# Kernel tuning notes

Measured on AMD Instinct MI355X. Metric: run time of the kernel, lower is better.

The kernel has to match this reference:

```python
import jax, jax.numpy as jnp
import numpy as np

DIM = 1024
MULTIPLE_OF = 256
NUM_EXPERTS = 8
TOP_K = 2
T = 2048  # flattened tokens


def _hidden_dim(dim: int, multiple_of: int) -> int:
    h = 4 * dim
    h = int(2 * h / 3)
    return multiple_of * ((h + multiple_of - 1) // multiple_of)

HIDDEN = _hidden_dim(DIM, MULTIPLE_OF)  # 2816


def setup_inputs() -> dict:
    key = jax.random.key(0)
    k_x, k_idx, k1, k2, k3 = jax.random.split(key, 5)
    x = jax.random.normal(k_x, (T, DIM), dtype=jnp.float32)
    expert_indices = jax.random.randint(k_idx, (T, TOP_K), 0, NUM_EXPERTS, dtype=jnp.int32)
    # parameters, matching nn.Parameter(torch.randn(E, H, D))
    w1 = jax.random.normal(k1, (NUM_EXPERTS, HIDDEN, DIM), dtype=jnp.float32)
    w2 = jax.random.normal(k2, (NUM_EXPERTS, HIDDEN, DIM), dtype=jnp.float32)
    w3 = jax.random.normal(k3, (NUM_EXPERTS, HIDDEN, DIM), dtype=jnp.float32)
    return {"x": x, "expert_indices": expert_indices, "w1": w1, "w2": w2, "w3": w3}


def reference(x, expert_indices, w1, w2, w3):
    # Same math as the torch module, but instead of materializing the
    # per-token gathered weights [T, A, H, D] (which the original does and
    # which blows up memory), we compute the SwiGLU FFN for ALL experts via
    # dense GEMMs and gather the selected experts' outputs per token.
    # Gather commutes with the per-expert linear maps, so math is identical.
    x1_all = jax.nn.silu(jnp.einsum('td,ehd->teh', x, w1))  # [T, E, H]
    x3_all = jnp.einsum('td,ehd->teh', x, w3)               # [T, E, H]
    g_all = x1_all * x3_all                                  # [T, E, H]
    out_all = jnp.einsum('teh,ehd->ted', g_all, w2)          # [T, E, D]
    # select top_k experts per token -> [T, A, D]
    idx = expert_indices[:, :, None].astype(jnp.int32)       # [T, A, 1]
    return jnp.take_along_axis(out_all, idx, axis=1)
```

## Files before the change

### kernel.cpp

```cpp
#include <hip/hip_runtime.h>

#define NTOK 2048
#define NEXP 8
#define TOPK 2
#define NITEM 4096
#define DIM 1024
#define HID 2816
#define CAP 4096
#define LDP 72

typedef unsigned short u16;
typedef __bf16 bf16x8 __attribute__((ext_vector_type(8)));
typedef float f32x4 __attribute__((ext_vector_type(4)));

__device__ __forceinline__ u16 f2bf(float f) {
  unsigned u = __float_as_uint(f);
  return (u16)((u + 0x7FFFu + ((u >> 16) & 1u)) >> 16);
}
__device__ __forceinline__ unsigned pk2(float a, float b) {
  return (unsigned)f2bf(a) | ((unsigned)f2bf(b) << 16);
}
__device__ __forceinline__ void async16(const void* g, void* l) {
  __builtin_amdgcn_global_load_lds(
      (const __attribute__((address_space(1))) unsigned int*)g,
      (__attribute__((address_space(3))) unsigned int*)l, 16, 0, 0);
}
__device__ __forceinline__ const bf16x8* fragpA(const u16* base, int row, int ko) {
  int byte = ((row << 7) + (ko << 1)) ^ ((row & 7) << 4);
  return (const bf16x8*)((const char*)base + byte);
}
__device__ __forceinline__ const bf16x8* fragpB(const u16* base, int row, int kg) {
  int byte = (row << 6) + ((kg << 4) ^ (((row >> 1) & 3) << 4));
  return (const bf16x8*)((const char*)base + byte);
}
__device__ __forceinline__ void cvst8(const float4& a, const float4& b, void* dst) {
  union { __bf16 h[8]; uint4 q; } u;
  u.h[0] = (__bf16)a.x; u.h[1] = (__bf16)a.y; u.h[2] = (__bf16)a.z; u.h[3] = (__bf16)a.w;
  u.h[4] = (__bf16)b.x; u.h[5] = (__bf16)b.y; u.h[6] = (__bf16)b.z; u.h[7] = (__bf16)b.w;
  *(uint4*)dst = u.q;
}

__global__ void zero8(int* counts) {
  if (threadIdx.x < NEXP) counts[threadIdx.x] = 0;
}

__global__ void bucket(const int* __restrict__ ei, int* counts, int* lists) {
  int item = blockIdx.x * 256 + threadIdx.x;
  if (item < NITEM) {
    int e = ei[item] & 7;
    int pos = atomicAdd(&counts[e], 1);
    if (pos < CAP) lists[e * CAP + pos] = item;
  }
}

__global__ __launch_bounds__(256) void cvt8(const float* __restrict__ src,
                                            u16* __restrict__ dst, int n8) {
  int i = blockIdx.x * 256 + threadIdx.x;
  if (i >= n8) return;
  float4 v0 = *(const float4*)(src + (size_t)i * 8);
  float4 v1 = *(const float4*)(src + (size_t)i * 8 + 4);
  uint4 u;
  u.x = pk2(v0.x, v0.y); u.y = pk2(v0.z, v0.w);
  u.z = pk2(v1.x, v1.y); u.w = pk2(v1.z, v1.w);
  *(uint4*)(dst + (size_t)i * 8) = u;
}

__global__ __launch_bounds__(256) void tw2(const float* __restrict__ w2, u16* __restrict__ w2t) {
  __shared__ float tile[64][65];
  const int e = blockIdx.z;
  const int h0 = blockIdx.y * 64;
  const int d0 = blockIdx.x * 64;
  const int tid = threadIdx.x;
  const int r = tid >> 4, c = (tid & 15) * 4;
  const float* src = w2 + (size_t)e * HID * DIM;
#pragma unroll
  for (int p = 0; p < 4; ++p) {
    float4 v = *(const float4*)(src + (size_t)(h0 + p * 16 + r) * DIM + d0 + c);
    tile[p * 16 + r][c] = v.x;
    tile[p * 16 + r][c + 1] = v.y;
    tile[p * 16 + r][c + 2] = v.z;
    tile[p * 16 + r][c + 3] = v.w;
  }
  __syncthreads();
  u16* dst = w2t + (size_t)e * DIM * HID;
#pragma unroll
  for (int p = 0; p < 4; ++p) {
    int dd = p * 16 + r;
    uint2 pkv;
    pkv.x = pk2(tile[c][dd], tile[c + 1][dd]);
    pkv.y = pk2(tile[c + 2][dd], tile[c + 3][dd]);
    *(uint2*)(dst + (size_t)(d0 + dd) * HID + h0 + c) = pkv;
  }
}


__global__ __launch_bounds__(256, 2) void gemm1H(
    const u16* __restrict__ xb, const float* __restrict__ w1,
    const float* __restrict__ w3, const int* __restrict__ counts,
    const int* __restrict__ lists, u16* __restrict__ G) {
  __shared__ __align__(16) u16 As[2][256 * 32];
  __shared__ __align__(16) u16 B1s[2][64 * 32];
  __shared__ __align__(16) u16 B3s[2][64 * 32];
  __shared__ int toks[256];

  const int e = blockIdx.z;
  int cnt = counts[e];
  if ((unsigned)cnt > CAP) cnt = 0;
  const int m0 = blockIdx.y * 256;
  if (m0 >= cnt) return;
  const int n0 = blockIdx.x * 64;
  const int tid = threadIdx.x;

  {
    int r = m0 + tid;
    int it = lists[e * CAP + (r < cnt ? r : 0)];
    toks[tid] = ((unsigned)it < NITEM) ? it : 0;
  }
  __syncthreads();

  const int lane = tid & 63;
  const int wrow = (tid >> 6) * 64;
  const int lr = lane & 15;
  const int kg = lane >> 4;

  const int prow = tid >> 2;
  const int q = tid & 3;
  const int ascol = (q ^ ((prow >> 1) & 3)) * 8;
  const u16* xs[4];
#pragma unroll
  for (int p = 0; p < 4; ++p)
    xs[p] = xb + (size_t)(toks[p * 64 + prow] >> 1) * DIM + ascol;

  const int br = prow;
  const float* w1p = w1 + ((size_t)e * HID + n0 + br) * DIM + q * 8;
  const float* w3p = w3 + ((size_t)e * HID + n0 + br) * DIM + q * 8;
  const int bby = (br << 6) + ((q << 4) ^ (((br >> 1) & 3) << 4));

  float4 b1r[2][2], b3r[2][2];
  f32x4 acc1[4][4] = {};
  f32x4 acc3[4][4] = {};

#define KCL(k) ((k) < DIM ? (k) : (DIM - 32))
#define G1_LOADB(set, k)                                  \
  {                                                       \
    b1r[set][0] = *(const float4*)(w1p + (k));            \
    b1r[set][1] = *(const float4*)(w1p + (k) + 4);        \
    b3r[set][0] = *(const float4*)(w3p + (k));            \
    b3r[set][1] = *(const float4*)(w3p + (k) + 4);        \
  }
#define G1_STGA(buf, k)                                   \
  {                                                       \
    char* aD = (char*)As[buf] + tid * 16;                 \
    async16(xs[0] + (k), aD);                             \
    async16(xs[1] + (k), aD + 4096);                      \
    async16(xs[2] + (k), aD + 8192);                      \
    async16(xs[3] + (k), aD + 12288);                     \
  }
#define G1_WRITEB(buf, set)                                   \
  {                                                           \
    cvst8(b1r[set][0], b1r[set][1], (char*)B1s[buf] + bby);   \
    cvst8(b3r[set][0], b3r[set][1], (char*)B3s[buf] + bby);   \
  }
#define G1_COMP(cb)                                                          \
  {                                                                          \
    bf16x8 a[4];                                                             \
    _Pragma("unroll") for (int m = 0; m < 4; ++m)                            \
        a[m] = *fragpB(As[cb], wrow + m * 16 + lr, kg);                      \
    _Pragma("unroll") for (int n = 0; n < 4; ++n) {                          \
      bf16x8 b1 = *fragpB(B1s[cb], n * 16 + lr, kg);                         \
      bf16x8 b3 = *fragpB(B3s[cb], n * 16 + lr, kg);                         \
      _Pragma("unroll") for (int m = 0; m < 4; ++m) {                        \
        acc1[m][n] = __builtin_amdgcn_mfma_f32_16x16x32_bf16(a[m], b1, acc1[m][n], 0, 0, 0); \
        acc3[m][n] = __builtin_amdgcn_mfma_f32_16x16x32_bf16(a[m], b3, acc3[m][n], 0, 0, 0); \
      }                                                                      \
    }                                                                        \
  }
#define G1_ITER(i, cb)                                               \
  {                                                                  \
    G1_STGA(cb ^ 1, KCL(32 * ((i) + 1)));                            \
    G1_WRITEB(cb ^ 1, cb ^ 1);              \
    __builtin_amdgcn_sched_barrier(0);                               \
    G1_LOADB(cb, KCL(32 * ((i) + 2)));                               \
    __builtin_amdgcn_sched_barrier(0);                               \
    G1_COMP(cb);                                                     \
    asm volatile("s_waitcnt vmcnt(4) lgkmcnt(0)" ::: "memory");      \
    __builtin_amdgcn_sched_barrier(0);                               \
    __builtin_amdgcn_s_barrier();                                    \
    __builtin_amdgcn_sched_barrier(0);                               \
  }

  G1_LOADB(0, 0);
  __builtin_amdgcn_sched_barrier(0);
  G1_STGA(0, 0);
  __builtin_amdgcn_sched_barrier(0);
  G1_LOADB(1, 32);
  asm volatile("s_waitcnt vmcnt(4)" ::: "memory");
  __builtin_amdgcn_sched_barrier(0);
  G1_WRITEB(0, 0);
  asm volatile("s_waitcnt lgkmcnt(0)" ::: "memory");
  __builtin_amdgcn_sched_barrier(0);
  __builtin_amdgcn_s_barrier();
  __builtin_amdgcn_sched_barrier(0);

  for (int i = 0; i < 32; i += 2) {
    G1_ITER(i, 0);
    G1_ITER(i + 1, 1);
  }
#undef G1_ITER
#undef G1_COMP
#undef G1_WRITEB
#undef G1_STGA
#undef G1_LOADB
#undef KCL

#pragma unroll
  for (int m = 0; m < 4; ++m) {
#pragma unroll
    for (int r = 0; r < 4; ++r) {
      const int row = wrow + m * 16 + kg * 4 + r;
      if (m0 + row < cnt) {
        const int it = toks[row];
        u16* gp = G + (size_t)it * HID + n0 + lr;
#pragma unroll
        for (int n = 0; n < 4; ++n) {
          float v1 = acc1[m][n][r];
          float v3 = acc3[m][n][r];
          float s = v1 / (1.f + __expf(-v1)) * v3;
          gp[n * 16] = f2bf(s);
        }
      }
    }
  }
}

__global__ __launch_bounds__(256, 3) void gemm2F(
    const u16* __restrict__ G, const u16* __restrict__ w2t,
    const int* __restrict__ counts, const int* __restrict__ lists,
    float* __restrict__ out) {
  __shared__ __align__(16) u16 As[2][128 * 64];
  __shared__ __align__(16) u16 Bs[2][64 * 64];
  __shared__ int toks[128];

  const int e = blockIdx.z;
  int cnt = counts[e];
  if ((unsigned)cnt > CAP) cnt = 0;
  const int m0 = blockIdx.y * 128;
  if (m0 >= cnt) return;
  const int n0 = blockIdx.x * 64;
  const int tid = threadIdx.x;

  if (tid < 128) {
    int r = m0 + tid;
    int it = lists[e * CAP + (r < cnt ? r : 0)];
    toks[tid] = ((unsigned)it < NITEM) ? it : 0;
  }
  __syncthreads();

  const int lane = tid & 63;
  const int wid = tid >> 6;
  const int wr = (wid >> 1) * 64;
  const int wc = (wid & 1) * 32;
  const int lr = lane & 15;
  const int kg = lane >> 4;

  const int srow = tid >> 3;
  const int scol = ((tid & 7) ^ (srow & 7)) * 8;

  const u16* as0 = G + (size_t)toks[srow] * HID + scol;
  const u16* as1 = G + (size_t)toks[32 + srow] * HID + scol;
  const u16* as2 = G + (size_t)toks[64 + srow] * HID + scol;
  const u16* as3 = G + (size_t)toks[96 + srow] * HID + scol;
  const u16* bs0 = w2t + ((size_t)e * DIM + n0 + srow) * HID + scol;
  const u16* bs1 = bs0 + (size_t)32 * HID;

  f32x4 acc[4][2] = {};

#define STG2(buf, k)                          \
  {                                           \
    char* aD = (char*)As[buf] + tid * 16;     \
    char* bD = (char*)Bs[buf] + tid * 16;     \
    async16(as0 + (k), aD);                   \
    async16(as1 + (k), aD + 4096);            \
    async16(as2 + (k), aD + 8192);            \
    async16(as3 + (k), aD + 12288);           \
    async16(bs0 + (k), bD);                   \
    async16(bs1 + (k), bD + 4096);            \
  }

  STG2(0, 0);
  __syncthreads();

  int cur = 0;
  for (int k0 = 0; k0 < HID; k0 += 64) {
    if (k0 + 64 < HID) STG2(cur ^ 1, k0 + 64);
    const u16* Ab = As[cur];
    const u16* Bb = Bs[cur];
#pragma unroll
    for (int kk = 0; kk < 2; ++kk) {
      const int ko = kk * 32 + kg * 8;
      bf16x8 a[4], b[2];
#pragma unroll
      for (int m = 0; m < 4; ++m) a[m] = *fragpA(Ab, wr + m * 16 + lr, ko);
#pragma unroll
      for (int n = 0; n < 2; ++n) b[n] = *fragpA(Bb, wc + n * 16 + lr, ko);
#pragma unroll
      for (int n = 0; n < 2; ++n)
#pragma unroll
        for (int m = 0; m < 4; ++m)
          acc[m][n] = __builtin_amdgcn_mfma_f32_16x16x32_bf16(a[m], b[n], acc[m][n], 0, 0, 0);
    }
    __syncthreads();
    cur ^= 1;
  }
#undef STG2

#pragma unroll
  for (int m = 0; m < 4; ++m) {
#pragma unroll
    for (int r = 0; r < 4; ++r) {
      const int row = wr + m * 16 + kg * 4 + r;
      if (m0 + row < cnt) {
        const int it = toks[row];
        float* op = out + (size_t)it * DIM + n0 + wc + lr;
#pragma unroll
        for (int n = 0; n < 2; ++n)
          op[n * 16] = acc[m][n][r];
      }
    }
  }
}


__global__ __launch_bounds__(256, 2) void gemm1B(
    const float* __restrict__ x, const float* __restrict__ w1,
    const float* __restrict__ w3, const int* __restrict__ counts,
    const int* __restrict__ lists, u16* __restrict__ G) {
  __shared__ __align__(16) u16 As[128 * LDP];
  __shared__ __align__(16) u16 B1s[128 * LDP];
  __shared__ __align__(16) u16 B3s[128 * LDP];
  __shared__ int toks[128];

  const int e = blockIdx.z;
  int cnt = counts[e];
  if ((unsigned)cnt > CAP) cnt = 0;
  const int m0 = blockIdx.y * 128;
  if (m0 >= cnt) return;
  const int n0 = blockIdx.x * 128;
  const int tid = threadIdx.x;

  if (tid < 128) {
    int r = m0 + tid;
    int it = lists[e * CAP + (r < cnt ? r : 0)];
    toks[tid] = ((unsigned)it < NITEM) ? it : 0;
  }
  __syncthreads();

  const int lane = tid & 63;
  const int wr = ((tid >> 7) & 1) * 64;
  const int wc = ((tid >> 6) & 1) * 64;
  const int lr = lane & 15;
  const int kg = lane >> 4;
  const int arow = tid >> 3;
  const int c8 = (tid & 7) * 8;

  const float* xsrc[4];
#pragma unroll
  for (int p = 0; p < 4; ++p)
    xsrc[p] = x + (size_t)(toks[p * 32 + arow] >> 1) * DIM + c8;
  const float* w1p = w1 + ((size_t)e * HID + n0 + arow) * DIM + c8;
  const float* w3p = w3 + ((size_t)e * HID + n0 + arow) * DIM + c8;

  f32x4 acc1[4][4] = {};
  f32x4 acc3[4][4] = {};

  for (int k0 = 0; k0 < DIM; k0 += 64) {
#pragma unroll
    for (int p = 0; p < 4; ++p) {
      float4 v0 = *(const float4*)(xsrc[p] + k0);
      float4 v1 = *(const float4*)(xsrc[p] + k0 + 4);
      uint4 u;
      u.x = pk2(v0.x, v0.y); u.y = pk2(v0.z, v0.w);
      u.z = pk2(v1.x, v1.y); u.w = pk2(v1.z, v1.w);
      *(uint4*)&As[(p * 32 + arow) * LDP + c8] = u;
    }
#pragma unroll
    for (int p = 0; p < 4; ++p) {
      float4 v0 = *(const float4*)(w1p + (size_t)(p * 32) * DIM + k0);
      float4 v1 = *(const float4*)(w1p + (size_t)(p * 32) * DIM + k0 + 4);
      uint4 u;
      u.x = pk2(v0.x, v0.y); u.y = pk2(v0.z, v0.w);
      u.z = pk2(v1.x, v1.y); u.w = pk2(v1.z, v1.w);
      *(uint4*)&B1s[(p * 32 + arow) * LDP + c8] = u;
      v0 = *(const float4*)(w3p + (size_t)(p * 32) * DIM + k0);
      v1 = *(const float4*)(w3p + (size_t)(p * 32) * DIM + k0 + 4);
      u.x = pk2(v0.x, v0.y); u.y = pk2(v0.z, v0.w);
      u.z = pk2(v1.x, v1.y); u.w = pk2(v1.z, v1.w);
      *(uint4*)&B3s[(p * 32 + arow) * LDP + c8] = u;
    }
    __syncthreads();
#pragma unroll
    for (int kk = 0; kk < 2; ++kk) {
      const int ko = kk * 32 + kg * 8;
      bf16x8 a[4];
#pragma unroll
      for (int m = 0; m < 4; ++m)
        a[m] = *(const bf16x8*)&As[(wr + m * 16 + lr) * LDP + ko];
#pragma unroll
      for (int n = 0; n < 4; ++n) {
        bf16x8 b1 = *(const bf16x8*)&B1s[(wc + n * 16 + lr) * LDP + ko];
        bf16x8 b3 = *(const bf16x8*)&B3s[(wc + n * 16 + lr) * LDP + ko];
#pragma unroll
        for (int m = 0; m < 4; ++m) {
          acc1[m][n] = __builtin_amdgcn_mfma_f32_16x16x32_bf16(a[m], b1, acc1[m][n], 0, 0, 0);
          acc3[m][n] = __builtin_amdgcn_mfma_f32_16x16x32_bf16(a[m], b3, acc3[m][n], 0, 0, 0);
        }
      }
    }
    __syncthreads();
  }

#pragma unroll
  for (int m = 0; m < 4; ++m) {
#pragma unroll
    for (int r = 0; r < 4; ++r) {
      const int row = wr + m * 16 + kg * 4 + r;
      if (m0 + row < cnt) {
        const int it = toks[row];
        u16* gp = G + (size_t)it * HID + n0 + wc + lr;
#pragma unroll
        for (int n = 0; n < 4; ++n) {
          float v1 = acc1[m][n][r];
          float v3 = acc3[m][n][r];
          float s = v1 / (1.f + __expf(-v1)) * v3;
          gp[n * 16] = f2bf(s);
        }
      }
    }
  }
}

__global__ __launch_bounds__(256, 2) void gemm2B(
    const u16* __restrict__ G, const float* __restrict__ w2,
    const int* __restrict__ counts, const int* __restrict__ lists,
    float* __restrict__ out) {
  __shared__ __align__(16) u16 As[128 * LDP];
  __shared__ __align__(16) u16 Bs[128 * LDP];
  __shared__ int toks[128];

  const int e = blockIdx.z;
  int cnt = counts[e];
  if ((unsigned)cnt > CAP) cnt = 0;
  const int m0 = blockIdx.y * 128;
  if (m0 >= cnt) return;
  const int n0 = blockIdx.x * 128;
  const int tid = threadIdx.x;

  if (tid < 128) {
    int r = m0 + tid;
    int it = lists[e * CAP + (r < cnt ? r : 0)];
    toks[tid] = ((unsigned)it < NITEM) ? it : 0;
  }
  __syncthreads();

  const int lane = tid & 63;
  const int wr = ((tid >> 7) & 1) * 64;
  const int wc = ((tid >> 6) & 1) * 64;
  const int lr = lane & 15;
  const int kg = lane >> 4;
  const int arow = tid >> 3;
  const int c8 = (tid & 7) * 8;
  const int brow = tid >> 5;
  const int d4 = (tid & 31) * 4;

  const u16* asrc[4];
#pragma unroll
  for (int p = 0; p < 4; ++p)
    asrc[p] = G + (size_t)toks[p * 32 + arow] * HID + c8;
  const float* bsrc = w2 + ((size_t)e * HID) * DIM + n0 + d4;

  f32x4 acc[4][4] = {};

  for (int k0 = 0; k0 < HID; k0 += 64) {
#pragma unroll
    for (int p = 0; p < 4; ++p) {
      uint4 u = *(const uint4*)(asrc[p] + k0);
      *(uint4*)&As[(p * 32 + arow) * LDP + c8] = u;
    }
#pragma unroll
    for (int p = 0; p < 8; ++p) {
      const int hl = p * 8 + brow;
      float4 v = *(const float4*)(bsrc + (size_t)(k0 + hl) * DIM);
      Bs[(d4 + 0) * LDP + hl] = f2bf(v.x);
      Bs[(d4 + 1) * LDP + hl] = f2bf(v.y);
      Bs[(d4 + 2) * LDP + hl] = f2bf(v.z);
      Bs[(d4 + 3) * LDP + hl] = f2bf(v.w);
    }
    __syncthreads();
#pragma unroll
    for (int kk = 0; kk < 2; ++kk) {
      const int ko = kk * 32 + kg * 8;
      bf16x8 a[4];
#pragma unroll
      for (int m = 0; m < 4; ++m)
        a[m] = *(const bf16x8*)&As[(wr + m * 16 + lr) * LDP + ko];
#pragma unroll
      for (int n = 0; n < 4; ++n) {
        bf16x8 b = *(const bf16x8*)&Bs[(wc + n * 16 + lr) * LDP + ko];
#pragma unroll
        for (int m = 0; m < 4; ++m)
          acc[m][n] = __builtin_amdgcn_mfma_f32_16x16x32_bf16(a[m], b, acc[m][n], 0, 0, 0);
      }
    }
    __syncthreads();
  }

#pragma unroll
  for (int m = 0; m < 4; ++m) {
#pragma unroll
    for (int r = 0; r < 4; ++r) {
      const int row = wr + m * 16 + kg * 4 + r;
      if (m0 + row < cnt) {
        const int it = toks[row];
        float* op = out + (size_t)it * DIM + n0 + wc + lr;
#pragma unroll
        for (int n = 0; n < 4; ++n)
          op[n * 16] = acc[m][n][r];
      }
    }
  }
}

extern "C" void kernel_launch(void* const* d_in, const int* in_sizes, int n_in,
                              void* d_out, int out_size, void* d_ws, size_t ws_size,
                              hipStream_t stream) {
  (void)in_sizes; (void)n_in; (void)out_size;
  const float* x  = (const float*)d_in[0];
  const int*   ei = (const int*)d_in[1];
  const float* w1 = (const float*)d_in[2];
  const float* w2 = (const float*)d_in[3];
  const float* w3 = (const float*)d_in[4];
  float* out = (float*)d_out;

  char* ws = (char*)d_ws;

  const size_t oG = 0;
  const size_t oXB = 23068672u;
  const size_t oW2T = oXB + 4194304u;
  const size_t oCNT = oW2T + 46137344u;
  const size_t oLST = oCNT + 64u;
  const size_t needA = oLST + 131072u;

  if (ws_size >= needA) {
    u16* G      = (u16*)(ws + oG);
    u16* xb     = (u16*)(ws + oXB);
    u16* w2t    = (u16*)(ws + oW2T);
    int* counts = (int*)(ws + oCNT);
    int* lists  = (int*)(ws + oLST);

    zero8<<<1, 64, 0, stream>>>(counts);
    bucket<<<NITEM / 256, 256, 0, stream>>>(ei, counts, lists);
    cvt8<<<(NTOK * DIM / 8) / 256, 256, 0, stream>>>(x, xb, NTOK * DIM / 8);
    gemm1H<<<dim3(HID / 64, CAP / 256, NEXP), 256, 0, stream>>>(xb, w1, w3, counts, lists, G);
    tw2<<<dim3(DIM / 64, HID / 64, NEXP), 256, 0, stream>>>(w2, w2t);
    gemm2F<<<dim3(DIM / 64, CAP / 128, NEXP), 256, 0, stream>>>(G, w2t, counts, lists, out);
  } else {
    u16* G      = (u16*)ws;
    int* counts = (int*)(ws + 23068672u);
    int* lists  = (int*)(ws + 23068736u);

    zero8<<<1, 64, 0, stream>>>(counts);
    bucket<<<NITEM / 256, 256, 0, stream>>>(ei, counts, lists);
    gemm1B<<<dim3(HID / 128, CAP / 128, NEXP), 256, 0, stream>>>(x, w1, w3, counts, lists, G);
    gemm2B<<<dim3(DIM / 128, CAP / 128, NEXP), 256, 0, stream>>>(G, w2, counts, lists, out);
  }
}
```

Before: 211.4 us.

## Fuse w2 transpose-convert into second GEMM and triple-buffer first GEMM A tiles

```diff
diff --git a/kernel.cpp b/kernel.cpp
--- a/kernel.cpp
+++ b/kernel.cpp
@@ -65,50 +65,27 @@
   *(uint4*)(dst + (size_t)i * 8) = u;
 }
 
-__global__ __launch_bounds__(256) void tw2(const float* __restrict__ w2, u16* __restrict__ w2t) {
-  __shared__ float tile[64][65];
-  const int e = blockIdx.z;
-  const int h0 = blockIdx.y * 64;
-  const int d0 = blockIdx.x * 64;
-  const int tid = threadIdx.x;
-  const int r = tid >> 4, c = (tid & 15) * 4;
-  const float* src = w2 + (size_t)e * HID * DIM;
-#pragma unroll
-  for (int p = 0; p < 4; ++p) {
-    float4 v = *(const float4*)(src + (size_t)(h0 + p * 16 + r) * DIM + d0 + c);
-    tile[p * 16 + r][c] = v.x;
-    tile[p * 16 + r][c + 1] = v.y;
-    tile[p * 16 + r][c + 2] = v.z;
-    tile[p * 16 + r][c + 3] = v.w;
-  }
-  __syncthreads();
-  u16* dst = w2t + (size_t)e * DIM * HID;
-#pragma unroll
-  for (int p = 0; p < 4; ++p) {
-    int dd = p * 16 + r;
-    uint2 pkv;
-    pkv.x = pk2(tile[c][dd], tile[c + 1][dd]);
-    pkv.y = pk2(tile[c + 2][dd], tile[c + 3][dd]);
-    *(uint2*)(dst + (size_t)(d0 + dd) * HID + h0 + c) = pkv;
-  }
-}
-
-
-__global__ __launch_bounds__(256, 2) void gemm1H(
+
+__global__ __launch_bounds__(256, 2) void gemm1I(
     const u16* __restrict__ xb, const float* __restrict__ w1,
     const float* __restrict__ w3, const int* __restrict__ counts,
     const int* __restrict__ lists, u16* __restrict__ G) {
-  __shared__ __align__(16) u16 As[2][256 * 32];
+  __shared__ __align__(16) u16 As[3][256 * 32];
   __shared__ __align__(16) u16 B1s[2][64 * 32];
   __shared__ __align__(16) u16 B3s[2][64 * 32];
   __shared__ int toks[256];
 
-  const int e = blockIdx.z;
+  const int flat = blockIdx.x;
+  const int n_id = flat % 44;
+  const int t2 = flat / 44;
+  const int e = t2 & 7;
+  const int m_id = t2 >> 3;
+
   int cnt = counts[e];
   if ((unsigned)cnt > CAP) cnt = 0;
-  const int m0 = blockIdx.y * 256;
+  const int m0 = m_id * 256;
   if (m0 >= cnt) return;
-  const int n0 = blockIdx.x * 64;
+  const int n0 = n_id * 64;
   const int tid = threadIdx.x;
 
   {
@@ -161,40 +138,42 @@
     cvst8(b1r[set][0], b1r[set][1], (char*)B1s[buf] + bby);   \
     cvst8(b3r[set][0], b3r[set][1], (char*)B3s[buf] + bby);   \
   }
-#define G1_COMP(cb)                                                          \
+#define G1_COMP(ab, bb)                                                      \
   {                                                                          \
     bf16x8 a[4];                                                             \
     _Pragma("unroll") for (int m = 0; m < 4; ++m)                            \
-        a[m] = *fragpB(As[cb], wrow + m * 16 + lr, kg);                      \
+        a[m] = *fragpB(As[ab], wrow + m * 16 + lr, kg);                      \
     _Pragma("unroll") for (int n = 0; n < 4; ++n) {                          \
-      bf16x8 b1 = *fragpB(B1s[cb], n * 16 + lr, kg);                         \
-      bf16x8 b3 = *fragpB(B3s[cb], n * 16 + lr, kg);                         \
+      bf16x8 b1 = *fragpB(B1s[bb], n * 16 + lr, kg);                         \
+      bf16x8 b3 = *fragpB(B3s[bb], n * 16 + lr, kg);                         \
       _Pragma("unroll") for (int m = 0; m < 4; ++m) {                        \
         acc1[m][n] = __builtin_amdgcn_mfma_f32_16x16x32_bf16(a[m], b1, acc1[m][n], 0, 0, 0); \
         acc3[m][n] = __builtin_amdgcn_mfma_f32_16x16x32_bf16(a[m], b3, acc3[m][n], 0, 0, 0); \
       }                                                                      \
     }                                                                        \
   }
-#define G1_ITER(i, cb)                                               \
+#define G1_ITER(I, AC, AS2, BC, BW)                                  \
   {                                                                  \
-    G1_STGA(cb ^ 1, KCL(32 * ((i) + 1)));                            \
-    G1_WRITEB(cb ^ 1, cb ^ 1);              \
-    __builtin_amdgcn_sched_barrier(0);                               \
-    G1_LOADB(cb, KCL(32 * ((i) + 2)));                               \
-    __builtin_amdgcn_sched_barrier(0);                               \
-    G1_COMP(cb);                                                     \
-    asm volatile("s_waitcnt vmcnt(4) lgkmcnt(0)" ::: "memory");      \
+    G1_STGA(AS2, KCL(32 * ((I) + 2)));                               \
+    __builtin_amdgcn_sched_barrier(0);                               \
+    asm volatile("s_waitcnt vmcnt(4)" ::: "memory");                 \
+    __builtin_amdgcn_sched_barrier(0);                               \
+    G1_WRITEB(BW, BW);                                               \
+    G1_LOADB(BC, KCL(32 * ((I) + 2)));                               \
+    __builtin_amdgcn_sched_barrier(0);                               \
+    G1_COMP(AC, BC);                                                 \
+    asm volatile("s_waitcnt lgkmcnt(0)" ::: "memory");               \
     __builtin_amdgcn_sched_barrier(0);                               \
     __builtin_amdgcn_s_barrier();                                    \
     __builtin_amdgcn_sched_barrier(0);                               \
   }
 
   G1_LOADB(0, 0);
-  __builtin_amdgcn_sched_barrier(0);
   G1_STGA(0, 0);
-  __builtin_amdgcn_sched_barrier(0);
   G1_LOADB(1, 32);
-  asm volatile("s_waitcnt vmcnt(4)" ::: "memory");
+  G1_STGA(1, 32);
+  __builtin_amdgcn_sched_barrier(0);
+  asm volatile("s_waitcnt vmcnt(8)" ::: "memory");
   __builtin_amdgcn_sched_barrier(0);
   G1_WRITEB(0, 0);
   asm volatile("s_waitcnt lgkmcnt(0)" ::: "memory");
@@ -202,10 +181,16 @@
   __builtin_amdgcn_s_barrier();
   __builtin_amdgcn_sched_barrier(0);
 
-  for (int i = 0; i < 32; i += 2) {
-    G1_ITER(i, 0);
-    G1_ITER(i + 1, 1);
-  }
+  for (int i = 0; i < 30; i += 6) {
+    G1_ITER(i + 0, 0, 2, 0, 1);
+    G1_ITER(i + 1, 1, 0, 1, 0);
+    G1_ITER(i + 2, 2, 1, 0, 1);
+    G1_ITER(i + 3, 0, 2, 1, 0);
+    G1_ITER(i + 4, 1, 0, 0, 1);
+    G1_ITER(i + 5, 2, 1, 1, 0);
+  }
+  G1_ITER(30, 0, 2, 0, 1);
+  G1_ITER(31, 1, 0, 1, 0);
 #undef G1_ITER
 #undef G1_COMP
 #undef G1_WRITEB
@@ -233,23 +218,28 @@
   }
 }
 
-__global__ __launch_bounds__(256, 3) void gemm2F(
-    const u16* __restrict__ G, const u16* __restrict__ w2t,
+__global__ __launch_bounds__(256, 1) void gemm2T(
+    const u16* __restrict__ G, const float* __restrict__ w2,
     const int* __restrict__ counts, const int* __restrict__ lists,
     float* __restrict__ out) {
-  __shared__ __align__(16) u16 As[2][128 * 64];
+  __shared__ __align__(16) u16 As[2][256 * 64];
   __shared__ __align__(16) u16 Bs[2][64 * 64];
-  __shared__ int toks[128];
-
-  const int e = blockIdx.z;
+  __shared__ int toks[256];
+
+  const int flat = blockIdx.x;
+  const int n_id = flat & 15;
+  const int t2 = flat >> 4;
+  const int e = t2 & 7;
+  const int m_id = t2 >> 3;
+
   int cnt = counts[e];
   if ((unsigned)cnt > CAP) cnt = 0;
-  const int m0 = blockIdx.y * 128;
+  const int m0 = m_id * 256;
   if (m0 >= cnt) return;
-  const int n0 = blockIdx.x * 64;
+  const int n0 = n_id * 64;
   const int tid = threadIdx.x;
 
-  if (tid < 128) {
+  {
     int r = m0 + tid;
     int it = lists[e * CAP + (r < cnt ? r : 0)];
     toks[tid] = ((unsigned)it < NITEM) ? it : 0;
@@ -257,73 +247,116 @@
   __syncthreads();
 
   const int lane = tid & 63;
-  const int wid = tid >> 6;
-  const int wr = (wid >> 1) * 64;
-  const int wc = (wid & 1) * 32;
+  const int wrow = (tid >> 6) * 64;
   const int lr = lane & 15;
   const int kg = lane >> 4;
 
   const int srow = tid >> 3;
-  const int scol = ((tid & 7) ^ (srow & 7)) * 8;
-
-  const u16* as0 = G + (size_t)toks[srow] * HID + scol;
-  const u16* as1 = G + (size_t)toks[32 + srow] * HID + scol;
-  const u16* as2 = G + (size_t)toks[64 + srow] * HID + scol;
-  const u16* as3 = G + (size_t)toks[96 + srow] * HID + scol;
-  const u16* bs0 = w2t + ((size_t)e * DIM + n0 + srow) * HID + scol;
-  const u16* bs1 = bs0 + (size_t)32 * HID;
-
-  f32x4 acc[4][2] = {};
-
-#define STG2(buf, k)                          \
-  {                                           \
-    char* aD = (char*)As[buf] + tid * 16;     \
-    char* bD = (char*)Bs[buf] + tid * 16;     \
-    async16(as0 + (k), aD);                   \
-    async16(as1 + (k), aD + 4096);            \
-    async16(as2 + (k), aD + 8192);            \
-    async16(as3 + (k), aD + 12288);           \
-    async16(bs0 + (k), bD);                   \
-    async16(bs1 + (k), bD + 4096);            \
-  }
-
-  STG2(0, 0);
-  __syncthreads();
-
-  int cur = 0;
-  for (int k0 = 0; k0 < HID; k0 += 64) {
-    if (k0 + 64 < HID) STG2(cur ^ 1, k0 + 64);
-    const u16* Ab = As[cur];
-    const u16* Bb = Bs[cur];
-#pragma unroll
-    for (int kk = 0; kk < 2; ++kk) {
-      const int ko = kk * 32 + kg * 8;
-      bf16x8 a[4], b[2];
-#pragma unroll
-      for (int m = 0; m < 4; ++m) a[m] = *fragpA(Ab, wr + m * 16 + lr, ko);
-#pragma unroll
-      for (int n = 0; n < 2; ++n) b[n] = *fragpA(Bb, wc + n * 16 + lr, ko);
-#pragma unroll
-      for (int n = 0; n < 2; ++n)
-#pragma unroll
-        for (int m = 0; m < 4; ++m)
-          acc[m][n] = __builtin_amdgcn_mfma_f32_16x16x32_bf16(a[m], b[n], acc[m][n], 0, 0, 0);
-    }
-    __syncthreads();
-    cur ^= 1;
-  }
-#undef STG2
+  const int c = tid & 7;
+  const int scol = ((c ^ (srow & 7)) * 8);
+  const u16* as[8];
+#pragma unroll
+  for (int p = 0; p < 8; ++p)
+    as[p] = G + (size_t)toks[p * 32 + srow] * HID + scol;
+
+  const int h = tid & 63;
+  const int tg = tid >> 6;
+  const float* w2p = w2 + ((size_t)e * HID + h) * DIM + n0 + tg * 4;
+
+  float4 bq[2][4];
+  f32x4 acc[4][4] = {};
+
+#define KCL2(k) ((k) < HID ? (k) : (HID - 64))
+#define G2_LOADB(set, k)                                           \
+  {                                                                \
+    _Pragma("unroll") for (int qq = 0; qq < 4; ++qq)               \
+        bq[set][qq] = *(const float4*)(w2p + (size_t)(k) * DIM + qq * 16); \
+  }
+#define G2_STGA(buf, k)                                            \
+  {                                                                \
+    char* aD = (char*)As[buf] + tid * 16;                          \
+    _Pragma("unroll") for (int p = 0; p < 8; ++p)                  \
+        async16(as[p] + (k), aD + p * 4096);                       \
+  }
+#define G2_WB1(buf, set, qq, jj, val)                                        \
+  {                                                                          \
+    int d_ = tg * 4 + (qq) * 16 + (jj);                                      \
+    int by_ = ((d_ << 7) + (h << 1)) ^ ((d_ & 7) << 4);                      \
+    *(u16*)((char*)Bs[buf] + by_) = f2bf(val);                               \
+  }
+#define G2_WRITEB(buf, set)                                  \
+  {                                                          \
+    _Pragma("unroll") for (int qq = 0; qq < 4; ++qq) {       \
+      G2_WB1(buf, set, qq, 0, bq[set][qq].x);                \
+      G2_WB1(buf, set, qq, 1, bq[set][qq].y);                \
+      G2_WB1(buf, set, qq, 2, bq[set][qq].z);                \
+      G2_WB1(buf, set, qq, 3, bq[set][qq].w);                \
+    }                                                        \
+  }
+#define G2_COMP(cb)                                                          \
+  {                                                                          \
+    _Pragma("unroll") for (int kk = 0; kk < 2; ++kk) {                       \
+      const int ko = kk * 32 + kg * 8;                                       \
+      bf16x8 a[4], b[4];                                                     \
+      _Pragma("unroll") for (int m = 0; m < 4; ++m)                          \
+          a[m] = *fragpA(As[cb], wrow + m * 16 + lr, ko);                    \
+      _Pragma("unroll") for (int n = 0; n < 4; ++n)                          \
+          b[n] = *fragpA(Bs[cb], n * 16 + lr, ko);                           \
+      _Pragma("unroll") for (int n = 0; n < 4; ++n)                          \
+          _Pragma("unroll") for (int m = 0; m < 4; ++m)                      \
+              acc[m][n] = __builtin_amdgcn_mfma_f32_16x16x32_bf16(a[m], b[n], acc[m][n], 0, 0, 0); \
+    }                                                                        \
+  }
+#define G2_IT(I, PB, CB)                                             \
+  {                                                                  \
+    G2_STGA(PB, KCL2(64 * ((I) + 1)));                               \
+    __builtin_amdgcn_sched_barrier(0);                               \
+    asm volatile("s_waitcnt vmcnt(8)" ::: "memory");                 \
+    __builtin_amdgcn_sched_barrier(0);                               \
+    G2_WRITEB(PB, PB);                                               \
+    G2_LOADB(CB, KCL2(64 * ((I) + 2)));                              \
+    __builtin_amdgcn_sched_barrier(0);                               \
+    G2_COMP(CB);                                                     \
+    asm volatile("s_waitcnt vmcnt(4) lgkmcnt(0)" ::: "memory");      \
+    __builtin_amdgcn_sched_barrier(0);                               \
+    __builtin_amdgcn_s_barrier();                                    \
+    __builtin_amdgcn_sched_barrier(0);                               \
+  }
+
+  G2_LOADB(0, 0);
+  G2_STGA(0, 0);
+  G2_LOADB(1, 64);
+  __builtin_amdgcn_sched_barrier(0);
+  asm volatile("s_waitcnt vmcnt(4)" ::: "memory");
+  __builtin_amdgcn_sched_barrier(0);
+  G2_WRITEB(0, 0);
+  asm volatile("s_waitcnt lgkmcnt(0)" ::: "memory");
+  __builtin_amdgcn_sched_barrier(0);
+  __builtin_amdgcn_s_barrier();
+  __builtin_amdgcn_sched_barrier(0);
+
+  for (int i = 0; i < 44; i += 2) {
+    G2_IT(i, 1, 0);
+    G2_IT(i + 1, 0, 1);
+  }
+#undef G2_IT
+#undef G2_COMP
+#undef G2_WRITEB
+#undef G2_WB1
+#undef G2_STGA
+#undef G2_LOADB
+#undef KCL2
 
 #pragma unroll
   for (int m = 0; m < 4; ++m) {
 #pragma unroll
     for (int r = 0; r < 4; ++r) {
-      const int row = wr + m * 16 + kg * 4 + r;
+      const int row = wrow + m * 16 + kg * 4 + r;
       if (m0 + row < cnt) {
         const int it = toks[row];
-        float* op = out + (size_t)it * DIM + n0 + wc + lr;
-#pragma unroll
-        for (int n = 0; n < 2; ++n)
+        float* op = out + (size_t)it * DIM + n0 + lr;
+#pragma unroll
+        for (int n = 0; n < 4; ++n)
           op[n * 16] = acc[m][n][r];
       }
     }
@@ -545,24 +578,21 @@
 
   const size_t oG = 0;
   const size_t oXB = 23068672u;
-  const size_t oW2T = oXB + 4194304u;
-  const size_t oCNT = oW2T + 46137344u;
+  const size_t oCNT = oXB + 4194304u;
   const size_t oLST = oCNT + 64u;
   const size_t needA = oLST + 131072u;
 
   if (ws_size >= needA) {
     u16* G      = (u16*)(ws + oG);
     u16* xb     = (u16*)(ws + oXB);
-    u16* w2t    = (u16*)(ws + oW2T);
     int* counts = (int*)(ws + oCNT);
     int* lists  = (int*)(ws + oLST);
 
     zero8<<<1, 64, 0, stream>>>(counts);
     bucket<<<NITEM / 256, 256, 0, stream>>>(ei, counts, lists);
     cvt8<<<(NTOK * DIM / 8) / 256, 256, 0, stream>>>(x, xb, NTOK * DIM / 8);
-    gemm1H<<<dim3(HID / 64, CAP / 256, NEXP), 256, 0, stream>>>(xb, w1, w3, counts, lists, G);
-    tw2<<<dim3(DIM / 64, HID / 64, NEXP), 256, 0, stream>>>(w2, w2t);
-    gemm2F<<<dim3(DIM / 64, CAP / 128, NEXP), 256, 0, stream>>>(G, w2t, counts, lists, out);
+    gemm1I<<<44 * 8 * 16, 256, 0, stream>>>(xb, w1, w3, counts, lists, G);
+    gemm2T<<<16 * 8 * 16, 256, 0, stream>>>(G, w2, counts, lists, out);
   } else {
     u16* G      = (u16*)ws;
     int* counts = (int*)(ws + 23068672u);
```

Measured after the change: 247.7 us. 1.17x slower.

## Triple-buffer A tiles in gemm1 and flatten grids to interleave experts

Applied to the files above, without the earlier changes.

```diff
diff --git a/kernel.cpp b/kernel.cpp
--- a/kernel.cpp
+++ b/kernel.cpp
@@ -94,21 +94,26 @@
 }
 
 
-__global__ __launch_bounds__(256, 2) void gemm1H(
+__global__ __launch_bounds__(256, 2) void gemm1I(
     const u16* __restrict__ xb, const float* __restrict__ w1,
     const float* __restrict__ w3, const int* __restrict__ counts,
     const int* __restrict__ lists, u16* __restrict__ G) {
-  __shared__ __align__(16) u16 As[2][256 * 32];
+  __shared__ __align__(16) u16 As[3][256 * 32];
   __shared__ __align__(16) u16 B1s[2][64 * 32];
   __shared__ __align__(16) u16 B3s[2][64 * 32];
   __shared__ int toks[256];
 
-  const int e = blockIdx.z;
+  const int flat = blockIdx.x;
+  const int n_id = flat % 44;
+  const int t2 = flat / 44;
+  const int e = t2 & 7;
+  const int m_id = t2 >> 3;
+
   int cnt = counts[e];
   if ((unsigned)cnt > CAP) cnt = 0;
-  const int m0 = blockIdx.y * 256;
+  const int m0 = m_id * 256;
   if (m0 >= cnt) return;
-  const int n0 = blockIdx.x * 64;
+  const int n0 = n_id * 64;
   const int tid = threadIdx.x;
 
   {
@@ -161,40 +166,42 @@
     cvst8(b1r[set][0], b1r[set][1], (char*)B1s[buf] + bby);   \
     cvst8(b3r[set][0], b3r[set][1], (char*)B3s[buf] + bby);   \
   }
-#define G1_COMP(cb)                                                          \
+#define G1_COMP(ab, bb)                                                      \
   {                                                                          \
     bf16x8 a[4];                                                             \
     _Pragma("unroll") for (int m = 0; m < 4; ++m)                            \
-        a[m] = *fragpB(As[cb], wrow + m * 16 + lr, kg);                      \
+        a[m] = *fragpB(As[ab], wrow + m * 16 + lr, kg);                      \
     _Pragma("unroll") for (int n = 0; n < 4; ++n) {                          \
-      bf16x8 b1 = *fragpB(B1s[cb], n * 16 + lr, kg);                         \
-      bf16x8 b3 = *fragpB(B3s[cb], n * 16 + lr, kg);                         \
+      bf16x8 b1 = *fragpB(B1s[bb], n * 16 + lr, kg);                         \
+      bf16x8 b3 = *fragpB(B3s[bb], n * 16 + lr, kg);                         \
       _Pragma("unroll") for (int m = 0; m < 4; ++m) {                        \
         acc1[m][n] = __builtin_amdgcn_mfma_f32_16x16x32_bf16(a[m], b1, acc1[m][n], 0, 0, 0); \
         acc3[m][n] = __builtin_amdgcn_mfma_f32_16x16x32_bf16(a[m], b3, acc3[m][n], 0, 0, 0); \
       }                                                                      \
     }                                                                        \
   }
-#define G1_ITER(i, cb)                                               \
+#define G1_ITER(I, AC, AS2, BC, BW)                                  \
   {                                                                  \
-    G1_STGA(cb ^ 1, KCL(32 * ((i) + 1)));                            \
-    G1_WRITEB(cb ^ 1, cb ^ 1);              \
+    G1_STGA(AS2, KCL(32 * ((I) + 2)));                               \
     __builtin_amdgcn_sched_barrier(0);                               \
-    G1_LOADB(cb, KCL(32 * ((i) + 2)));                               \
+    asm volatile("s_waitcnt vmcnt(4)" ::: "memory");                 \
     __builtin_amdgcn_sched_barrier(0);                               \
-    G1_COMP(cb);                                                     \
-    asm volatile("s_waitcnt vmcnt(4) lgkmcnt(0)" ::: "memory");      \
+    G1_WRITEB(BW, BW);                                               \
+    G1_LOADB(BC, KCL(32 * ((I) + 2)));                               \
+    __builtin_amdgcn_sched_barrier(0);                               \
+    G1_COMP(AC, BC);                                                 \
+    asm volatile("s_waitcnt lgkmcnt(0)" ::: "memory");               \
     __builtin_amdgcn_sched_barrier(0);                               \
     __builtin_amdgcn_s_barrier();                                    \
     __builtin_amdgcn_sched_barrier(0);                               \
   }
 
   G1_LOADB(0, 0);
+  G1_STGA(0, 0);
+  G1_LOADB(1, 32);
+  G1_STGA(1, 32);
   __builtin_amdgcn_sched_barrier(0);
-  G1_STGA(0, 0);
-  __builtin_amdgcn_sched_barrier(0);
-  G1_LOADB(1, 32);
-  asm volatile("s_waitcnt vmcnt(4)" ::: "memory");
+  asm volatile("s_waitcnt vmcnt(8)" ::: "memory");
   __builtin_amdgcn_sched_barrier(0);
   G1_WRITEB(0, 0);
   asm volatile("s_waitcnt lgkmcnt(0)" ::: "memory");
@@ -202,10 +209,16 @@
   __builtin_amdgcn_s_barrier();
   __builtin_amdgcn_sched_barrier(0);
 
-  for (int i = 0; i < 32; i += 2) {
-    G1_ITER(i, 0);
-    G1_ITER(i + 1, 1);
-  }
+  for (int i = 0; i < 30; i += 6) {
+    G1_ITER(i + 0, 0, 2, 0, 1);
+    G1_ITER(i + 1, 1, 0, 1, 0);
+    G1_ITER(i + 2, 2, 1, 0, 1);
+    G1_ITER(i + 3, 0, 2, 1, 0);
+    G1_ITER(i + 4, 1, 0, 0, 1);
+    G1_ITER(i + 5, 2, 1, 1, 0);
+  }
+  G1_ITER(30, 0, 2, 0, 1);
+  G1_ITER(31, 1, 0, 1, 0);
 #undef G1_ITER
 #undef G1_COMP
 #undef G1_WRITEB
@@ -241,12 +254,17 @@
   __shared__ __align__(16) u16 Bs[2][64 * 64];
   __shared__ int toks[128];
 
-  const int e = blockIdx.z;
+  const int flat = blockIdx.x;
+  const int n_id = flat & 15;
+  const int t2 = flat >> 4;
+  const int e = t2 & 7;
+  const int m_id = t2 >> 3;
+
   int cnt = counts[e];
   if ((unsigned)cnt > CAP) cnt = 0;
-  const int m0 = blockIdx.y * 128;
+  const int m0 = m_id * 128;
   if (m0 >= cnt) return;
-  const int n0 = blockIdx.x * 64;
+  const int n0 = n_id * 64;
   const int tid = threadIdx.x;
 
   if (tid < 128) {
@@ -560,9 +578,9 @@
     zero8<<<1, 64, 0, stream>>>(counts);
     bucket<<<NITEM / 256, 256, 0, stream>>>(ei, counts, lists);
     cvt8<<<(NTOK * DIM / 8) / 256, 256, 0, stream>>>(x, xb, NTOK * DIM / 8);
-    gemm1H<<<dim3(HID / 64, CAP / 256, NEXP), 256, 0, stream>>>(xb, w1, w3, counts, lists, G);
+    gemm1I<<<44 * 8 * 16, 256, 0, stream>>>(xb, w1, w3, counts, lists, G);
     tw2<<<dim3(DIM / 64, HID / 64, NEXP), 256, 0, stream>>>(w2, w2t);
-    gemm2F<<<dim3(DIM / 64, CAP / 128, NEXP), 256, 0, stream>>>(G, w2t, counts, lists, out);
+    gemm2F<<<16 * 8 * 32, 256, 0, stream>>>(G, w2t, counts, lists, out);
   } else {
     u16* G      = (u16*)ws;
     int* counts = (int*)(ws + 23068672u);
```

Measured after the change: 199.4 us (median of 2 runs). -5.7%, faster.

## Fuse w2 transpose into gemm1 launch and flatten grids for tile ordering

Applied to the files above, without the earlier changes.

```diff
diff --git a/kernel.cpp b/kernel.cpp
--- a/kernel.cpp
+++ b/kernel.cpp
@@ -65,51 +65,62 @@
   *(uint4*)(dst + (size_t)i * 8) = u;
 }
 
-__global__ __launch_bounds__(256) void tw2(const float* __restrict__ w2, u16* __restrict__ w2t) {
-  __shared__ float tile[64][65];
-  const int e = blockIdx.z;
-  const int h0 = blockIdx.y * 64;
-  const int d0 = blockIdx.x * 64;
-  const int tid = threadIdx.x;
-  const int r = tid >> 4, c = (tid & 15) * 4;
-  const float* src = w2 + (size_t)e * HID * DIM;
-#pragma unroll
-  for (int p = 0; p < 4; ++p) {
-    float4 v = *(const float4*)(src + (size_t)(h0 + p * 16 + r) * DIM + d0 + c);
-    tile[p * 16 + r][c] = v.x;
-    tile[p * 16 + r][c + 1] = v.y;
-    tile[p * 16 + r][c + 2] = v.z;
-    tile[p * 16 + r][c + 3] = v.w;
-  }
-  __syncthreads();
-  u16* dst = w2t + (size_t)e * DIM * HID;
-#pragma unroll
-  for (int p = 0; p < 4; ++p) {
-    int dd = p * 16 + r;
-    uint2 pkv;
-    pkv.x = pk2(tile[c][dd], tile[c + 1][dd]);
-    pkv.y = pk2(tile[c + 2][dd], tile[c + 3][dd]);
-    *(uint2*)(dst + (size_t)(d0 + dd) * HID + h0 + c) = pkv;
-  }
-}
-
-
-__global__ __launch_bounds__(256, 2) void gemm1H(
+
+__global__ __launch_bounds__(256, 3) void g1tw(
     const u16* __restrict__ xb, const float* __restrict__ w1,
-    const float* __restrict__ w3, const int* __restrict__ counts,
-    const int* __restrict__ lists, u16* __restrict__ G) {
+    const float* __restrict__ w3, const float* __restrict__ w2,
+    const int* __restrict__ counts, const int* __restrict__ lists,
+    u16* __restrict__ G, u16* __restrict__ w2t) {
   __shared__ __align__(16) u16 As[2][256 * 32];
   __shared__ __align__(16) u16 B1s[2][64 * 32];
   __shared__ __align__(16) u16 B3s[2][64 * 32];
   __shared__ int toks[256];
 
-  const int e = blockIdx.z;
+  const int flat = blockIdx.x;
+  const int tid = threadIdx.x;
+
+  if (flat >= 5632) {
+    float(*tile)[65] = reinterpret_cast<float(*)[65]>(As);
+    const int t = flat - 5632;
+    const int dx = t & 15;
+    const int t2 = t >> 4;
+    const int hy = t2 % 44;
+    const int e = t2 / 44;
+    const int h0 = hy * 64;
+    const int d0 = dx * 64;
+    const int r = tid >> 4, c = (tid & 15) * 4;
+    const float* src = w2 + (size_t)e * HID * DIM;
+#pragma unroll
+    for (int p = 0; p < 4; ++p) {
+      float4 v = *(const float4*)(src + (size_t)(h0 + p * 16 + r) * DIM + d0 + c);
+      tile[p * 16 + r][c] = v.x;
+      tile[p * 16 + r][c + 1] = v.y;
+      tile[p * 16 + r][c + 2] = v.z;
+      tile[p * 16 + r][c + 3] = v.w;
+    }
+    __syncthreads();
+    u16* dst = w2t + (size_t)e * DIM * HID;
+#pragma unroll
+    for (int p = 0; p < 4; ++p) {
+      int dd = p * 16 + r;
+      uint2 pkv;
+      pkv.x = pk2(tile[c][dd], tile[c + 1][dd]);
+      pkv.y = pk2(tile[c + 2][dd], tile[c + 3][dd]);
+      *(uint2*)(dst + (size_t)(d0 + dd) * HID + h0 + c) = pkv;
+    }
+    return;
+  }
+
+  const int n_id = flat % 44;
+  const int t2g = flat / 44;
+  const int m_id = t2g & 15;
+  const int e = t2g >> 4;
+
   int cnt = counts[e];
   if ((unsigned)cnt > CAP) cnt = 0;
-  const int m0 = blockIdx.y * 256;
+  const int m0 = m_id * 256;
   if (m0 >= cnt) return;
-  const int n0 = blockIdx.x * 64;
-  const int tid = threadIdx.x;
+  const int n0 = n_id * 64;
 
   {
     int r = m0 + tid;
@@ -241,12 +252,17 @@
   __shared__ __align__(16) u16 Bs[2][64 * 64];
   __shared__ int toks[128];
 
-  const int e = blockIdx.z;
+  const int flat = blockIdx.x;
+  const int n_id = flat & 15;
+  const int t2 = flat >> 4;
+  const int e = t2 & 7;
+  const int m_id = t2 >> 3;
+
   int cnt = counts[e];
   if ((unsigned)cnt > CAP) cnt = 0;
-  const int m0 = blockIdx.y * 128;
+  const int m0 = m_id * 128;
   if (m0 >= cnt) return;
-  const int n0 = blockIdx.x * 64;
+  const int n0 = n_id * 64;
   const int tid = threadIdx.x;
 
   if (tid < 128) {
@@ -560,9 +576,8 @@
     zero8<<<1, 64, 0, stream>>>(counts);
     bucket<<<NITEM / 256, 256, 0, stream>>>(ei, counts, lists);
     cvt8<<<(NTOK * DIM / 8) / 256, 256, 0, stream>>>(x, xb, NTOK * DIM / 8);
-    gemm1H<<<dim3(HID / 64, CAP / 256, NEXP), 256, 0, stream>>>(xb, w1, w3, counts, lists, G);
-    tw2<<<dim3(DIM / 64, HID / 64, NEXP), 256, 0, stream>>>(w2, w2t);
-    gemm2F<<<dim3(DIM / 64, CAP / 128, NEXP), 256, 0, stream>>>(G, w2t, counts, lists, out);
+    g1tw<<<11264, 256, 0, stream>>>(xb, w1, w3, w2, counts, lists, G, w2t);
+    gemm2F<<<16 * 8 * 32, 256, 0, stream>>>(G, w2t, counts, lists, out);
   } else {
     u16* G      = (u16*)ws;
     int* counts = (int*)(ws + 23068672u);
```

Measured after the change: 699.2 us. 3.31x slower.
